# Kernel optimization log

Hardware: AMD Instinct MI355X
Metric: run time of the kernel (lower is better)

Reference implementation:

```python
import jax, jax.numpy as jnp
import numpy as np

N_QUBITS = 8
N_PAIRS = 4
PAIRS = [(2 * p, 2 * p + 1) for p in range(N_PAIRS)]
STRENGTH = 0.8
DIM = 2 ** N_QUBITS


def _apply_1q_full(st, G, q):
    # st: (2,)*n complex64 state, G: [2,2] gate on qubit q (qubit 0 = most significant)
    out = jnp.tensordot(G, st, axes=([1], [q]))
    return jnp.moveaxis(out, 0, q)


def _apply_ctrl_full(st, G, c, t):
    # controlled-G: apply G on target axis t only where control axis c == 1
    s0 = jnp.take(st, 0, axis=c)
    s1 = jnp.take(st, 1, axis=c)
    t2 = t if t < c else t - 1
    s1 = jnp.moveaxis(jnp.tensordot(G, s1, axes=([1], [t2])), 0, t2)
    return jnp.stack([s0, s1], axis=c)


def _entangled_base():
    # |0...0> -> H on q1, partial CNOT (controlled-RX(pi*strength)) on (q1,q2) per pair
    st = jnp.zeros((2,) * N_QUBITS, jnp.complex64).at[(0,) * N_QUBITS].set(1.0)
    H = jnp.array([[1.0, 1.0], [1.0, -1.0]], jnp.complex64) / np.float32(np.sqrt(2.0))
    th = np.float32(np.pi * STRENGTH)
    c, s = np.float32(np.cos(th / 2)), np.float32(np.sin(th / 2))
    RX = jnp.array([[c, -1j * s], [-1j * s, c]], jnp.complex64)
    for q1, q2 in PAIRS:
        st = _apply_1q_full(st, H, q1)
        st = _apply_ctrl_full(st, RX, q1, q2)
    return st.reshape(-1)


def _rx(theta):
    # RX(theta) = [[cos t/2, -i sin t/2], [-i sin t/2, cos t/2]], batched over theta shape
    cz = jnp.cos(0.5 * theta).astype(jnp.complex64)
    sz = (-1j) * jnp.sin(0.5 * theta).astype(jnp.complex64)
    return jnp.stack([jnp.stack([cz, sz], -1), jnpp_stack_fix(sz, cz)], -2) if False else jnp.stack([jnp.stack([cz, sz], -1), jnp.stack([sz, cz], -1)], -2)


def _rz(theta):
    ph = (0.5j) * theta.astype(jnp.complex64)
    e0, e1 = jnp.exp(-ph), jnp.exp(ph)
    z = jnp.zeros_like(e0)
    return jnp.stack([jnp.stack([e0, z], -1), jnp.stack([z, e1], -1)], -2)


def _quantum_scores(k_states):
    # k_states: [B,S,2*n_qubits] -> expected pair-agreement score [B,S]
    B, S, _ = k_states.shape
    k = k_states.reshape(B, S, N_QUBITS, 2)
    eye = jnp.eye(2, dtype=jnp.complex64)
    st = jnp.broadcast_to(_entangled_base(), (B, S, DIM))  # fresh entangled register per (b,j)
    for q in range(N_QUBITS):
        th_x, th_z = k[:, :, q, 0], k[:, :, q, 1]
        Gx = jnp.where((th_x > 0)[..., None, None], _rx(th_x), eye)
        Gz = jnp.where((th_z > 0)[..., None, None], _rz(th_z), eye)
        G = jnp.einsum('bsij,bsjk->bsik', Gz, Gx)  # RX applied first, then RZ
        L = 2 ** q
        R = DIM // (2 * L)
        stv = st.reshape(B, S, L, 2, R)
        st = jnp.einsum('bsij,bsljr->bslir', G, stv).reshape(B, S, DIM)
    probs = (st.real ** 2 + st.imag ** 2).reshape((B, S) + (2,) * N_QUBITS)
    score = jnp.zeros((B, S), probs.dtype)
    for q1, q2 in PAIRS:
        axes = tuple(2 + a for a in range(N_QUBITS) if a not in (q1, q2))
        marg = probs.sum(axis=axes)  # [B,S,2,2] joint marginal of the pair
        score = score + marg[..., 0, 0] + marg[..., 1, 1]  # P(measure equal)
    return score / N_PAIRS


def reference(query, key, value, Wq, bq, Wk, bk, Wv, bv, Wo, bo):
    q_states = query @ Wq + bq  # computed as in original forward (unused by scores)
    k_states = key @ Wk + bk    # [B,S,2*n_qubits]
    v_states = value @ Wv + bv  # [B,S,d_model]
    B, S, _ = k_states.shape
    score = _quantum_scores(k_states)  # [B,S]; deterministic expected agreement
    # original loop makes score[b,i,j] independent of i under independent per-(b,i,j) sims
    attn = jnp.broadcast_to(score[:, None, :], (B, S, S))
    w = jax.nn.softmax(attn, axis=-1)
    out = jnp.einsum('bij,bjd->bid', w, v_states)
    return out @ Wo + bo


def setup_inputs() -> dict:
    rng = jax.random.key(0)
    ks = jax.random.split(rng, 8)
    B, S, D = 8, 2048, 512
    nq2 = 2 * N_QUBITS
    f = jax.random.normal
    return {
        'query': f(ks[0], (B, S, D), jnp.float32),
        'key': f(ks[1], (B, S, D), jnp.float32),
        'value': f(ks[2], (B, S, D), jnp.float32),
        'Wq': f(ks[3], (D, nq2), jnp.float32) * 0.05,
        'bq': jnp.zeros((nq2,), jnp.float32),
        'Wk': f(ks[4], (D, nq2), jnp.float32) * 0.05,
        'bk': jnp.zeros((nq2,), jnp.float32),
        'Wv': f(ks[5], (D, D), jnp.float32) * 0.05,
        'bv': jnp.zeros((D,), jnp.float32),
        'Wo': f(ks[6], (D, D), jnp.float32) * 0.05,
        'bo': jnp.zeros((D,), jnp.float32),
    }
```

## Files before the change

### kernel.cpp

```cpp
#include <hip/hip_runtime.h>
#include <math.h>

#define DEV __device__ __forceinline__

struct C2 { float x, y; };
DEV C2 cmul(C2 a, C2 b){ return {a.x*b.x - a.y*b.y, a.x*b.y + a.y*b.x}; }
DEV C2 cadd(C2 a, C2 b){ return {a.x+b.x, a.y+b.y}; }
DEV C2 cscale(C2 a, float s){ return {a.x*s, a.y*s}; }
DEV C2 cnegi(C2 a){ return {a.y, -a.x}; }

__global__ __launch_bounds__(512, 4) void k_score_wsum(const float* __restrict__ key,
                                                       const float* __restrict__ Wk,
                                                       const float* __restrict__ bk,
                                                       const float* __restrict__ value,
                                                       float* __restrict__ partial,
                                                       float* __restrict__ partialw)
{
    const int c = blockIdx.x;
    const int b = blockIdx.y;
    const int t = threadIdx.x;
    const int lane = t & 63;
    const int wv   = t >> 6;
    const int h    = wv & 1;
    const int pr   = wv >> 1;
    const int base = b * 2048 + c * 32;
    const int wrow0 = pr * 8;

    __shared__ float  kslds[2][32][16];
    __shared__ float4 red[8][128];
    __shared__ float  wsums[4];

    float4 wk[4][4];
    #pragma unroll
    for (int jj = 0; jj < 4; ++jj) {
        const float4* w0 = (const float4*)(Wk + (h * 256 + 4 * lane + jj) * 16);
        #pragma unroll
        for (int q = 0; q < 4; ++q) wk[jj][q] = w0[q];
    }
    const float c0 = 0.30901699437494745f;
    const float s0 = 0.9510565162951535f;

    const float4* kp = (const float4*)(key + (size_t)(base + wrow0) * 512);
    float4 cur = kp[h * 64 + lane];
    #pragma unroll
    for (int j = 0; j < 8; ++j) {
        float4 nx;
        if (j < 7) nx = kp[(j + 1) * 128 + h * 64 + lane];
        float el[4] = {cur.x, cur.y, cur.z, cur.w};
        float acc[16];
        #pragma unroll
        for (int k = 0; k < 16; ++k) acc[k] = 0.f;
        #pragma unroll
        for (int jj = 0; jj < 4; ++jj) {
            #pragma unroll
            for (int q = 0; q < 4; ++q) {
                acc[4*q+0] = fmaf(el[jj], wk[jj][q].x, acc[4*q+0]);
                acc[4*q+1] = fmaf(el[jj], wk[jj][q].y, acc[4*q+1]);
                acc[4*q+2] = fmaf(el[jj], wk[jj][q].z, acc[4*q+2]);
                acc[4*q+3] = fmaf(el[jj], wk[jj][q].w, acc[4*q+3]);
            }
        }
        #pragma unroll
        for (int s = 0; s < 4; ++s) {
            const int m = 1 << s;
            const int bbit = (lane >> s) & 1;
            #pragma unroll
            for (int jj = 0; jj < (16 >> (s + 1)); ++jj) {
                float send = bbit ? acc[2*jj] : acc[2*jj+1];
                float keep = bbit ? acc[2*jj+1] : acc[2*jj];
                acc[jj] = keep + __shfl_xor(send, m);
            }
        }
        float ks = acc[0];
        ks += __shfl_xor(ks, 16);
        ks += __shfl_xor(ks, 32);
        if (lane < 16) kslds[h][wrow0 + j][lane] = ks;
        cur = nx;
    }

    const int vrow0 = wrow0 + h * 4;
    const float4* vp = (const float4*)(value + (size_t)(base + vrow0) * 512);
    float4 vreg[8];
    #pragma unroll
    for (int j = 0; j < 4; ++j) {
        vreg[2*j]   = vp[j * 128 + lane];
        vreg[2*j+1] = vp[j * 128 + 64 + lane];
    }
    __syncthreads();

    const int p  = (lane >> 3) & 3;
    const int jr = lane & 7;
    float4 k0 = *(const float4*)&kslds[0][wrow0 + jr][4 * p];
    float4 k1 = *(const float4*)&kslds[1][wrow0 + jr][4 * p];
    float4 bk4 = ((const float4*)bk)[p];
    float ax = k0.x + k1.x + bk4.x, az = k0.y + k1.y + bk4.y;
    float bx = k0.z + k1.z + bk4.z, bz = k0.w + k1.w + bk4.w;
    float cxa = 1.f, sxa = 0.f; if (ax > 0.f){ sxa = __sinf(0.5f*ax); cxa = __cosf(0.5f*ax); }
    float cpa = 1.f, spa = 0.f; if (az > 0.f){ spa = __sinf(0.5f*az); cpa = __cosf(0.5f*az); }
    float cxb = 1.f, sxb = 0.f; if (bx > 0.f){ sxb = __sinf(0.5f*bx); cxb = __cosf(0.5f*bx); }
    float cpb = 1.f, spb = 0.f; if (bz > 0.f){ spb = __sinf(0.5f*bz); cpb = __cosf(0.5f*bz); }
    C2 A00{cpa*cxa, -spa*cxa}, A01{-spa*sxa, -cpa*sxa};
    C2 A10{spa*sxa, -cpa*sxa}, A11{ cpa*cxa,  spa*cxa};
    C2 B00{cpb*cxb, -spb*cxb}, B01{-spb*sxb, -cpb*sxb};
    C2 B10{spb*sxb, -cpb*sxb}, B11{ cpb*cxb,  spb*cxb};
    C2 u = cadd(cmul(B00, cadd(A00, cscale(A01, c0))),
                cscale(cnegi(cmul(A01, B01)), s0));
    C2 v = cadd(cmul(B10, cadd(A10, cscale(A11, c0))),
                cscale(cnegi(cmul(A11, B11)), s0));
    float ps = u.x*u.x + u.y*u.y + v.x*v.x + v.y*v.y;
    ps += __shfl_xor(ps, 8);
    ps += __shfl_xor(ps, 16);
    float w_all = __expf(ps * 0.125f);

    if (h == 0) {
        float sw = w_all;
        sw += __shfl_xor(sw, 1); sw += __shfl_xor(sw, 2); sw += __shfl_xor(sw, 4);
        if (lane == 0) wsums[pr] = sw;
    }

    float4 aA = {0.f,0.f,0.f,0.f}, aB = {0.f,0.f,0.f,0.f};
    #pragma unroll
    for (int j = 0; j < 4; ++j) {
        float wj = __shfl(w_all, h * 4 + j);
        float4 v0 = vreg[2*j], v1 = vreg[2*j+1];
        aA.x = fmaf(wj, v0.x, aA.x); aA.y = fmaf(wj, v0.y, aA.y);
        aA.z = fmaf(wj, v0.z, aA.z); aA.w = fmaf(wj, v0.w, aA.w);
        aB.x = fmaf(wj, v1.x, aB.x); aB.y = fmaf(wj, v1.y, aB.y);
        aB.z = fmaf(wj, v1.z, aB.z); aB.w = fmaf(wj, v1.w, aB.w);
    }
    red[wv][lane] = aA;
    red[wv][64 + lane] = aB;
    __syncthreads();
    if (t < 128) {
        float4 q0 = red[0][t], q1 = red[1][t], q2 = red[2][t], q3 = red[3][t];
        float4 q4 = red[4][t], q5 = red[5][t], q6 = red[6][t], q7 = red[7][t];
        float4 o = { q0.x+q1.x+q2.x+q3.x+q4.x+q5.x+q6.x+q7.x,
                     q0.y+q1.y+q2.y+q3.y+q4.y+q5.y+q6.y+q7.y,
                     q0.z+q1.z+q2.z+q3.z+q4.z+q5.z+q6.z+q7.z,
                     q0.w+q1.w+q2.w+q3.w+q4.w+q5.w+q6.w+q7.w };
        ((float4*)partial)[((size_t)b * 64 + c) * 128 + t] = o;
    }
    if (t == 0)
        partialw[b * 64 + c] = wsums[0] + wsums[1] + wsums[2] + wsums[3];
}

__global__ __launch_bounds__(256) void k_ctx(const float* __restrict__ partial,
                                             const float* __restrict__ partialw,
                                             const float* __restrict__ Wv,
                                             const float* __restrict__ bv,
                                             float* __restrict__ ctx)
{
    int dt = blockIdx.x, b = blockIdx.y, t = threadIdx.x;
    __shared__ float4 red4[2][128];
    __shared__ float  vb[512];
    __shared__ float  red[256];
    __shared__ float  invS;

    if (t < 64) {
        float s = partialw[b * 64 + t];
        s += __shfl_xor(s, 1);  s += __shfl_xor(s, 2);
        s += __shfl_xor(s, 4);  s += __shfl_xor(s, 8);
        s += __shfl_xor(s, 16); s += __shfl_xor(s, 32);
        if (t == 0) invS = 1.f / s;
    }
    const int col4 = t & 127, cg = t >> 7;
    const float4* pp4 = (const float4*)partial
                      + ((size_t)b * 64 + cg * 32) * 128 + col4;
    float4 a = {0.f, 0.f, 0.f, 0.f};
    #pragma unroll 8
    for (int cc = 0; cc < 32; ++cc) {
        float4 v = pp4[(size_t)cc * 128];
        a.x += v.x; a.y += v.y; a.z += v.z; a.w += v.w;
    }
    red4[cg][col4] = a;
    __syncthreads();
    if (t < 128) {
        float4 q0 = red4[0][t], q1 = red4[1][t];
        float is = invS;
        vb[4*t+0] = (q0.x + q1.x) * is;
        vb[4*t+1] = (q0.y + q1.y) * is;
        vb[4*t+2] = (q0.z + q1.z) * is;
        vb[4*t+3] = (q0.w + q1.w) * is;
    }
    __syncthreads();

    int dl = t & 63, q = t >> 6;
    int d = dt * 64 + dl;
    const float* x  = vb + q * 128;
    const float* Wc = Wv + (size_t)(q * 128) * 512 + d;
    float acc = 0.f;
    #pragma unroll 8
    for (int e = 0; e < 128; ++e) acc = fmaf(x[e], Wc[(size_t)e * 512], acc);
    red[t] = acc; __syncthreads();
    if (t < 64)
        ctx[b * 512 + dt * 64 + t] = red[t] + red[t+64] + red[t+128] + red[t+192]
                                   + bv[dt * 64 + t];
}

__global__ __launch_bounds__(256) void k_frow(const float* __restrict__ ctx,
                                              const float* __restrict__ Wo,
                                              const float* __restrict__ bo,
                                              float* __restrict__ frow)
{
    int dt = blockIdx.x, b = blockIdx.y, t = threadIdx.x;
    __shared__ float xs[512];
    __shared__ float red[256];

    xs[t]       = ctx[b * 512 + t];
    xs[t + 256] = ctx[b * 512 + 256 + t];
    __syncthreads();

    int dl = t & 63, q = t >> 6;
    int d = dt * 64 + dl;
    const float* x  = xs + q * 128;
    const float* Wc = Wo + (size_t)(q * 128) * 512 + d;
    float acc = 0.f;
    #pragma unroll 8
    for (int e = 0; e < 128; ++e) acc = fmaf(x[e], Wc[(size_t)e * 512], acc);
    red[t] = acc; __syncthreads();
    if (t < 64)
        frow[b * 512 + dt * 64 + t] = red[t] + red[t+64] + red[t+128] + red[t+192]
                                    + bo[dt * 64 + t];
}

__global__ __launch_bounds__(256) void k_bcast(const float* __restrict__ frow,
                                               float* __restrict__ out)
{
    int s = blockIdx.x, b = blockIdx.y, t = threadIdx.x;
    const int col4 = t & 127, h = t >> 7;
    float4 val = ((const float4*)frow)[b * 128 + col4];
    float4* o4 = (float4*)out
               + ((size_t)b * 2048 + s * 32 + h * 16) * 128 + col4;
    #pragma unroll
    for (int r = 0; r < 16; ++r) o4[(size_t)r * 128] = val;
}

extern "C" void kernel_launch(void* const* d_in, const int* in_sizes, int n_in,
                              void* d_out, int out_size, void* d_ws, size_t ws_size,
                              hipStream_t stream) {
    const float* key   = (const float*)d_in[1];
    const float* value = (const float*)d_in[2];
    const float* Wk    = (const float*)d_in[5];
    const float* bk    = (const float*)d_in[6];
    const float* Wv    = (const float*)d_in[7];
    const float* bv    = (const float*)d_in[8];
    const float* Wo    = (const float*)d_in[9];
    const float* bo    = (const float*)d_in[10];
    float* out = (float*)d_out;
    float* ws  = (float*)d_ws;

    float* partial  = ws;
    float* partialw = ws + 262144;
    float* ctx      = ws + 262656;
    float* frow     = ws + 266752;

    k_score_wsum<<<dim3(64, 8), 512, 0, stream>>>(key, Wk, bk, value,
                                                  partial, partialw);
    k_ctx <<<dim3(8, 8),  256, 0, stream>>>(partial, partialw, Wv, bv, ctx);
    k_frow<<<dim3(8, 8),  256, 0, stream>>>(ctx, Wo, bo, frow);
    k_bcast<<<dim3(64, 8), 256, 0, stream>>>(frow, out);
}
```

Baseline: 170.2 us.

## Fuse context GEMV, output projection and broadcast into one tail kernel

Replaces the three tail kernels (Wv projection, Wo projection, row broadcast) with a single kernel in which each block recomputes the reduced context and both GEMVs, then writes its slice of output rows. This removes two kernel launches and the global round trips of the intermediate ctx/frow vectors. In exchange every block redundantly reads both weight matrices and the partial sums, and the large broadcast write is issued by fewer threads, which may reduce write throughput.

```diff
diff --git a/kernel.cpp b/kernel.cpp
--- a/kernel.cpp
+++ b/kernel.cpp
@@ -144,95 +144,75 @@
         partialw[b * 64 + c] = wsums[0] + wsums[1] + wsums[2] + wsums[3];
 }
 
-__global__ __launch_bounds__(256) void k_ctx(const float* __restrict__ partial,
-                                             const float* __restrict__ partialw,
-                                             const float* __restrict__ Wv,
-                                             const float* __restrict__ bv,
-                                             float* __restrict__ ctx)
+__global__ __launch_bounds__(512) void k_tail(const float* __restrict__ partial,
+                                              const float* __restrict__ partialw,
+                                              const float* __restrict__ Wv,
+                                              const float* __restrict__ bv,
+                                              const float* __restrict__ Wo,
+                                              const float* __restrict__ bo,
+                                              float* __restrict__ out)
 {
-    int dt = blockIdx.x, b = blockIdx.y, t = threadIdx.x;
-    __shared__ float4 red4[2][128];
-    __shared__ float  vb[512];
-    __shared__ float  red[256];
-    __shared__ float  invS;
+    const int sl = blockIdx.x;
+    const int b  = blockIdx.y;
+    const int t  = threadIdx.x;
+
+    __shared__ float cbuf[512];
+    __shared__ float xbuf[512];
+    __shared__ float frl[512];
+    __shared__ float sS;
 
     if (t < 64) {
         float s = partialw[b * 64 + t];
         s += __shfl_xor(s, 1);  s += __shfl_xor(s, 2);
         s += __shfl_xor(s, 4);  s += __shfl_xor(s, 8);
         s += __shfl_xor(s, 16); s += __shfl_xor(s, 32);
-        if (t == 0) invS = 1.f / s;
-    }
-    const int col4 = t & 127, cg = t >> 7;
-    const float4* pp4 = (const float4*)partial
-                      + ((size_t)b * 64 + cg * 32) * 128 + col4;
-    float4 a = {0.f, 0.f, 0.f, 0.f};
-    #pragma unroll 8
-    for (int cc = 0; cc < 32; ++cc) {
-        float4 v = pp4[(size_t)cc * 128];
-        a.x += v.x; a.y += v.y; a.z += v.z; a.w += v.w;
-    }
-    red4[cg][col4] = a;
-    __syncthreads();
-    if (t < 128) {
-        float4 q0 = red4[0][t], q1 = red4[1][t];
-        float is = invS;
-        vb[4*t+0] = (q0.x + q1.x) * is;
-        vb[4*t+1] = (q0.y + q1.y) * is;
-        vb[4*t+2] = (q0.z + q1.z) * is;
-        vb[4*t+3] = (q0.w + q1.w) * is;
-    }
-    __syncthreads();
-
-    int dl = t & 63, q = t >> 6;
-    int d = dt * 64 + dl;
-    const float* x  = vb + q * 128;
-    const float* Wc = Wv + (size_t)(q * 128) * 512 + d;
-    float acc = 0.f;
-    #pragma unroll 8
-    for (int e = 0; e < 128; ++e) acc = fmaf(x[e], Wc[(size_t)e * 512], acc);
-    red[t] = acc; __syncthreads();
-    if (t < 64)
-        ctx[b * 512 + dt * 64 + t] = red[t] + red[t+64] + red[t+128] + red[t+192]
-                                   + bv[dt * 64 + t];
-}
-
-__global__ __launch_bounds__(256) void k_frow(const float* __restrict__ ctx,
-                                              const float* __restrict__ Wo,
-                                              const float* __restrict__ bo,
-                                              float* __restrict__ frow)
-{
-    int dt = blockIdx.x, b = blockIdx.y, t = threadIdx.x;
-    __shared__ float xs[512];
-    __shared__ float red[256];
-
-    xs[t]       = ctx[b * 512 + t];
-    xs[t + 256] = ctx[b * 512 + 256 + t];
-    __syncthreads();
-
-    int dl = t & 63, q = t >> 6;
-    int d = dt * 64 + dl;
-    const float* x  = xs + q * 128;
-    const float* Wc = Wo + (size_t)(q * 128) * 512 + d;
-    float acc = 0.f;
-    #pragma unroll 8
-    for (int e = 0; e < 128; ++e) acc = fmaf(x[e], Wc[(size_t)e * 512], acc);
-    red[t] = acc; __syncthreads();
-    if (t < 64)
-        frow[b * 512 + dt * 64 + t] = red[t] + red[t+64] + red[t+128] + red[t+192]
-                                    + bo[dt * 64 + t];
-}
-
-__global__ __launch_bounds__(256) void k_bcast(const float* __restrict__ frow,
-                                               float* __restrict__ out)
-{
-    int s = blockIdx.x, b = blockIdx.y, t = threadIdx.x;
-    const int col4 = t & 127, h = t >> 7;
-    float4 val = ((const float4*)frow)[b * 128 + col4];
-    float4* o4 = (float4*)out
-               + ((size_t)b * 2048 + s * 32 + h * 16) * 128 + col4;
-    #pragma unroll
-    for (int r = 0; r < 16; ++r) o4[(size_t)r * 128] = val;
+        if (t == 0) sS = 1.f / s;
+    }
+
+    {
+        float cs = 0.f;
+        const float* pp = partial + (size_t)b * 32768 + t;
+        #pragma unroll 8
+        for (int cc = 0; cc < 64; ++cc) cs += pp[(size_t)cc * 512];
+        cbuf[t] = cs;
+    }
+    __syncthreads();
+    const float invS = sS;
+
+    {
+        float a0 = 0.f, a1 = 0.f, a2 = 0.f, a3 = 0.f;
+        #pragma unroll 4
+        for (int e = 0; e < 512; e += 4) {
+            a0 = fmaf(cbuf[e],   Wv[(size_t)e * 512 + t],     a0);
+            a1 = fmaf(cbuf[e+1], Wv[(size_t)(e+1) * 512 + t], a1);
+            a2 = fmaf(cbuf[e+2], Wv[(size_t)(e+2) * 512 + t], a2);
+            a3 = fmaf(cbuf[e+3], Wv[(size_t)(e+3) * 512 + t], a3);
+        }
+        xbuf[t] = ((a0 + a1) + (a2 + a3)) * invS + bv[t];
+    }
+    __syncthreads();
+
+    {
+        float a0 = 0.f, a1 = 0.f, a2 = 0.f, a3 = 0.f;
+        #pragma unroll 4
+        for (int e = 0; e < 512; e += 4) {
+            a0 = fmaf(xbuf[e],   Wo[(size_t)e * 512 + t],     a0);
+            a1 = fmaf(xbuf[e+1], Wo[(size_t)(e+1) * 512 + t], a1);
+            a2 = fmaf(xbuf[e+2], Wo[(size_t)(e+2) * 512 + t], a2);
+            a3 = fmaf(xbuf[e+3], Wo[(size_t)(e+3) * 512 + t], a3);
+        }
+        frl[t] = ((a0 + a1) + (a2 + a3)) + bo[t];
+    }
+    __syncthreads();
+
+    {
+        const int col4 = t & 127, rg = t >> 7;
+        float4 val = ((const float4*)frl)[col4];
+        float4* o4 = (float4*)out
+                   + ((size_t)b * 2048 + sl * 256 + rg * 64) * 128 + col4;
+        #pragma unroll 8
+        for (int r = 0; r < 64; ++r) o4[(size_t)r * 128] = val;
+    }
 }
 
 extern "C" void kernel_launch(void* const* d_in, const int* in_sizes, int n_in,
@@ -251,12 +231,9 @@
 
     float* partial  = ws;
     float* partialw = ws + 262144;
-    float* ctx      = ws + 262656;
-    float* frow     = ws + 266752;
 
     k_score_wsum<<<dim3(64, 8), 512, 0, stream>>>(key, Wk, bk, value,
                                                   partial, partialw);
-    k_ctx <<<dim3(8, 8),  256, 0, stream>>>(partial, partialw, Wv, bv, ctx);
-    k_frow<<<dim3(8, 8),  256, 0, stream>>>(ctx, Wo, bo, frow);
-    k_bcast<<<dim3(64, 8), 256, 0, stream>>>(frow, out);
+    k_tail      <<<dim3(8, 8),  512, 0, stream>>>(partial, partialw,
+                                                  Wv, bv, Wo, bo, out);
 }
```

Result: slower. 189.7 us (+11.5%).
